# Optimization experiments

Hardware: AMD Instinct MI355X
Metric: run time of the kernel (lower is better)

## Reference

```python
import jax, jax.numpy as jnp
import numpy as np

NEG_SLOPE = 0.2


def gat_layer(x, adj, W, a_src, a_dst):
    # x: (C, in_dim), adj: (C, C) 0/1, W: (in_dim, H*D), a_src/a_dst: (H, D)
    C = x.shape[0]
    H, D = a_src.shape
    h = (x @ W).reshape(C, H, D)            # (C, H, D)
    hh = jnp.transpose(h, (1, 0, 2))        # (H, C, D)
    asrc = jnp.einsum('hcd,hd->hc', hh, a_src)  # (H, C)
    adst = jnp.einsum('hcd,hd->hc', hh, a_dst)  # (H, C)
    e = asrc[:, :, None] + adst[:, None, :]     # (H, C, C)
    e = jax.nn.leaky_relu(e, NEG_SLOPE)
    e = jnp.where(adj[None, :, :] == 0, -jnp.inf, e)
    attn = jax.nn.softmax(e, axis=-1)           # (H, C, C)
    out = jnp.einsum('hij,hjd->hid', attn, hh)  # (H, C, D)
    return jnp.transpose(out, (1, 0, 2)).reshape(C, H * D)


def setup_inputs() -> dict:
    key = jax.random.key(0)
    ks = jax.random.split(key, 12)
    B, doc_dim = 1024, 768
    C, label_dim = 4096, 768
    hidden, H = 512, 4
    D = hidden // H  # 128

    doc_x = jax.random.normal(ks[0], (B, doc_dim), dtype=jnp.float32)
    label_init = jax.random.normal(ks[1], (C, label_dim), dtype=jnp.float32)
    adj = jax.random.randint(ks[2], (C, C), 0, 2, dtype=jnp.int32)
    adj = adj.at[jnp.arange(C), jnp.arange(C)].set(1)  # self-loops

    def xavier(k, shape):
        fan_in, fan_out = shape[0], shape[1]
        lim = jnp.sqrt(6.0 / (fan_in + fan_out)).astype(jnp.float32)
        return jax.random.uniform(k, shape, jnp.float32, -lim, lim)

    W1 = xavier(ks[3], (label_dim, hidden))
    a_src1 = xavier(ks[4], (H, D))
    a_dst1 = xavier(ks[5], (H, D))
    W2 = xavier(ks[6], (hidden, hidden))
    a_src2 = xavier(ks[7], (H, D))
    a_dst2 = xavier(ks[8], (H, D))
    Wd = xavier(ks[9], (doc_dim, hidden))
    bd = jnp.zeros((hidden,), jnp.float32)
    return {"doc_x": doc_x, "label_init": label_init, "adj": adj,
            "W1": W1, "a_src1": a_src1, "a_dst1": a_dst1,
            "W2": W2, "a_src2": a_src2, "a_dst2": a_dst2,
            "Wd": Wd, "bd": bd}


def reference(doc_x, label_init, adj, W1, a_src1, a_dst1, W2, a_src2, a_dst2, Wd, bd):
    # doc_proj (dropout = identity in eval)
    doc_h = jax.nn.relu(doc_x @ Wd + bd)            # (B, hidden)
    # label encoder: GAT -> ELU -> GAT
    h = gat_layer(label_init, adj, W1, a_src1, a_dst1)
    h = jax.nn.elu(h)
    label_h = gat_layer(h, adj, W2, a_src2, a_dst2)  # (C, hidden)
    logits = doc_h @ label_h.T                      # (B, C)
    return logits
```

## Files before the change

### kernel.cpp

```cpp
#include <hip/hip_runtime.h>
#include <hip/hip_bf16.h>
#include <math.h>

#define BDOCS   1024
#define CNODES  4096
#define INDIM   768
#define HID     512
#define NHEAD   4
#define HDIM    128
#define NEG_SLOPE 0.2f

#define KSPLIT  8
#define JPER    (CNODES / KSPLIT)
#define NCH     (JPER / 32)

typedef __attribute__((ext_vector_type(8))) short short8;
typedef __attribute__((ext_vector_type(4))) float f32x4;

__device__ __forceinline__ float lrelu(float x) { return x > 0.f ? x : NEG_SLOPE * x; }

__device__ __forceinline__ short f2bf(float f) {
    union { float f; unsigned u; } v; v.f = f;
    unsigned r = (v.u + 0x7fff + ((v.u >> 16) & 1)) >> 16;
    return (short)r;
}
__device__ __forceinline__ float bf2f(short s) {
    union { float f; unsigned u; } v; v.u = ((unsigned)(unsigned short)s) << 16;
    return v.f;
}
__device__ __forceinline__ unsigned pk2(float a, float b) {
    union { float f; unsigned u; } x, y; x.f = a; y.f = b;
    unsigned lo = (x.u + 0x7fff + ((x.u >> 16) & 1)) >> 16;
    unsigned hi = (y.u + 0x7fff + ((y.u >> 16) & 1)) >> 16;
    return lo | (hi << 16);
}
__device__ __forceinline__ short hup(float f) {
    union { float f; unsigned u; } v; v.f = f;
    return (short)((v.u + 0x8000) >> 16);
}
__device__ __forceinline__ unsigned encf(float x) {
    union { float f; unsigned u; } v; v.f = x;
    return (v.u & 0x80000000u) ? ~v.u : (v.u | 0x80000000u);
}
__device__ __forceinline__ float decf(unsigned u) {
    union { float f; unsigned u; } v;
    v.u = (u & 0x80000000u) ? (u ^ 0x80000000u) : ~u;
    return v.f;
}

__device__ void frag_T_dev(const float* __restrict__ src, short* __restrict__ dst,
                           int N, int K, int jc, int nq, float (*tile)[132])
{
    const int t  = threadIdx.x;
    const int KC = K >> 5;
#pragma unroll
    for (int it = 0; it < 16; it++) {
        const int e = it * 256 + t;
        const int j = e >> 7, n = e & 127;
        tile[j][n] = src[(size_t)(jc * 32 + j) * N + nq * 128 + n];
    }
    __syncthreads();
#pragma unroll
    for (int s = 0; s < 2; s++) {
        const int item = s * 256 + t;
        const int nbl = item >> 6, lane = item & 63;
        const int nr = lane & 15, kq = lane >> 4;
        short8 v;
#pragma unroll
        for (int jr = 0; jr < 8; jr++)
            v[jr] = f2bf(tile[kq * 8 + jr][nbl * 16 + nr]);
        *(short8*)&dst[((size_t)((nq * 8 + nbl) * KC + jc) * 64 + lane) * 8] = v;
    }
}

__device__ void frag_A_dev(const float* __restrict__ src, short* __restrict__ dst,
                           int C, int rb, int cq, float (*tile)[132])
{
    const int t  = threadIdx.x;
    const int KC = C >> 5;
#pragma unroll
    for (int it = 0; it < 8; it++) {
        const int e = it * 256 + t;
        const int r = e >> 7, c = e & 127;
        tile[r][c] = src[(size_t)(rb * 16 + r) * C + cq * 128 + c];
    }
    __syncthreads();
    const int kcl = t >> 6, lane = t & 63;
    const int m = lane & 15, kq = lane >> 4;
    short8 v8;
#pragma unroll
    for (int j = 0; j < 8; j++) v8[j] = f2bf(tile[m][kcl * 32 + kq * 8 + j]);
    *(short8*)&dst[((size_t)(rb * KC + cq * 4 + kcl) * 64 + lane) * 8] = v8;
}

#define PREP_BLOCKS (65536 + 96 + 96 + 64 + 384 + 1536)
__global__ __launch_bounds__(256)
void prep_all(const int* __restrict__ adj, unsigned long long* __restrict__ adjb64,
              const float* __restrict__ Wd, short* __restrict__ Wdf,
              const float* __restrict__ W1, short* __restrict__ W1f,
              const float* __restrict__ W2, short* __restrict__ W2f,
              const float* __restrict__ doc_x, short* __restrict__ dxf,
              const float* __restrict__ label_init, short* __restrict__ lif,
              unsigned* __restrict__ MhEnc)
{
    __shared__ float tile[32][132];
    int b = blockIdx.x;
    if (b < 65536) {
        if (b == 0 && threadIdx.x < 16) MhEnc[threadIdx.x] = 0x007FFFFFu;
        const int t    = threadIdx.x;
        const int gw   = b * 4 + (t >> 6);
        const int lane = t & 63;
        const int i  = gw >> 6;
        const int j0 = (gw & 63) * 64;
        const int a  = adj[(size_t)i * CNODES + j0 + lane];
        const unsigned long long msk = __ballot(a != 0);
        if (lane == 0) adjb64[(size_t)i * 64 + (j0 >> 6)] = msk;
        return;
    }
    b -= 65536;
    if (b < 96)  { frag_T_dev(Wd, Wdf, HID, INDIM, b % 24, b / 24, tile); return; }
    b -= 96;
    if (b < 96)  { frag_T_dev(W1, W1f, HID, INDIM, b % 24, b / 24, tile); return; }
    b -= 96;
    if (b < 64)  { frag_T_dev(W2, W2f, HID, HID, b % 16, b / 16, tile); return; }
    b -= 64;
    if (b < 384) { frag_A_dev(doc_x, dxf, INDIM, b % 64, b / 64, tile); return; }
    b -= 384;
    frag_A_dev(label_init, lif, INDIM, b % 256, b / 256, tile);
}

template <int KC>
__global__ __launch_bounds__(64)
void gemm_hpre(const short* __restrict__ Af, const short* __restrict__ Bf,
               const float* __restrict__ a_src, const float* __restrict__ a_dst,
               short* __restrict__ hbTf, float* __restrict__ asrc, float* __restrict__ adst,
               unsigned* __restrict__ MhEncH)
{
    __shared__ __align__(16) short tileT[64][24];
    const int lane = threadIdx.x;
    const int mb   = blockIdx.x;
    const int h    = blockIdx.y >> 1;
    const int ch   = blockIdx.y & 1;
    const int i0   = mb * 16;

    f32x4 acc[4];
#pragma unroll
    for (int c = 0; c < 4; c++) acc[c] = (f32x4){0.f, 0.f, 0.f, 0.f};

    const short* ap = Af + (size_t)mb * KC * 512 + lane * 8;
    const short* bp = Bf + (size_t)(h * 8 + ch * 4) * KC * 512 + lane * 8;

#pragma unroll 2
    for (int kc = 0; kc < KC; kc++) {
        short8 a = *(const short8*)(ap + (size_t)kc * 512);
#pragma unroll
        for (int c = 0; c < 4; c++) {
            short8 bf = *(const short8*)(bp + ((size_t)c * KC + kc) * 512);
            acc[c] = __builtin_amdgcn_mfma_f32_16x16x32_bf16(a, bf, acc[c], 0, 0, 0);
        }
    }

    const int col = lane & 15, q4 = lane >> 4;

#pragma unroll
    for (int c = 0; c < 4; c++) {
        uint2 u;
        u.x = pk2(acc[c][0], acc[c][1]);
        u.y = pk2(acc[c][2], acc[c][3]);
        *(uint2*)&tileT[c * 16 + col][q4 * 4] = u;
    }
    __syncthreads();
    {
        const int jc = mb >> 1, khalf = mb & 1;
        const int nr = lane & 15, kq = lane >> 4;
        if ((kq >> 1) == khalf) {
#pragma unroll
            for (int cl = 0; cl < 4; cl++) {
                short8 v = *(const short8*)&tileT[cl * 16 + nr][(kq & 1) * 8];
                const int nbl = h * 8 + ch * 4 + cl;
                *(short8*)&hbTf[(((size_t)nbl * (CNODES / 32) + jc) * 64 + lane) * 8] = v;
            }
        }
    }

    float ssrc[4] = {}, sdst[4] = {};
#pragma unroll
    for (int c = 0; c < 4; c++) {
        const float vs = a_src[h * 128 + ch * 64 + c * 16 + col];
        const float vd = a_dst[h * 128 + ch * 64 + c * 16 + col];
#pragma unroll
        for (int r = 0; r < 4; r++) {
            ssrc[r] += acc[c][r] * vs;
            sdst[r] += acc[c][r] * vd;
        }
    }
#pragma unroll
    for (int mask = 1; mask <= 8; mask <<= 1)
#pragma unroll
        for (int r = 0; r < 4; r++) {
            ssrc[r] += __shfl_xor(ssrc[r], mask);
            sdst[r] += __shfl_xor(sdst[r], mask);
        }
    if (col == 0) {
#pragma unroll
        for (int r = 0; r < 4; r++) {
            const int row = i0 + q4 * 4 + r;
            atomicAdd(asrc + h * CNODES + row, ssrc[r]);
            atomicAdd(adst + h * CNODES + row, sdst[r]);
        }
    }
    float wmax = fmaxf(fmaxf(sdst[0], sdst[1]), fmaxf(sdst[2], sdst[3]));
    wmax = fmaxf(wmax, __shfl_xor(wmax, 16));
    wmax = fmaxf(wmax, __shfl_xor(wmax, 32));
    if (lane == 0) atomicMax(MhEncH + h * 2 + ch, encf(wmax));
}

template <int KC>
__global__ __launch_bounds__(64)
void gemm_doc(const short* __restrict__ Af, const short* __restrict__ Bf,
              const float* __restrict__ bias, short* __restrict__ dhf)
{
    __shared__ __align__(16) short tile[16][32];
    const int lane = threadIdx.x;
    const int mb = blockIdx.x;
    const int ng = blockIdx.y;

    f32x4 acc[2];
#pragma unroll
    for (int c = 0; c < 2; c++) acc[c] = (f32x4){0.f, 0.f, 0.f, 0.f};

    const short* ap = Af + (size_t)mb * KC * 512 + lane * 8;
    const short* bp = Bf + (size_t)(ng * 2) * KC * 512 + lane * 8;

#pragma unroll 2
    for (int kc = 0; kc < KC; kc++) {
        short8 a = *(const short8*)(ap + (size_t)kc * 512);
#pragma unroll
        for (int c = 0; c < 2; c++) {
            short8 bf = *(const short8*)(bp + ((size_t)c * KC + kc) * 512);
            acc[c] = __builtin_amdgcn_mfma_f32_16x16x32_bf16(a, bf, acc[c], 0, 0, 0);
        }
    }

    const int col = lane & 15, q4 = lane >> 4;
#pragma unroll
    for (int c = 0; c < 2; c++)
#pragma unroll
        for (int r = 0; r < 4; r++) {
            float v = fmaxf(acc[c][r] + bias[ng * 32 + c * 16 + col], 0.f);
            tile[q4 * 4 + r][c * 16 + col] = f2bf(v);
        }
    __syncthreads();
    const int m = lane & 15, kq = lane >> 4;
    short8 v = *(const short8*)&tile[m][kq * 8];
    *(short8*)&dhf[(((size_t)mb * 16 + ng) * 64 + lane) * 8] = v;
}

template <int KC>
__global__ __launch_bounds__(64)
void gemm_frag(const short* __restrict__ Af, const short* __restrict__ Bf,
               float* __restrict__ Cmat, int N)
{
    const int lane = threadIdx.x;
    const int mb0  = blockIdx.x * 2;
    const int ng   = blockIdx.y;

    f32x4 acc[2][4];
#pragma unroll
    for (int f = 0; f < 2; f++)
#pragma unroll
        for (int c = 0; c < 4; c++) acc[f][c] = (f32x4){0.f, 0.f, 0.f, 0.f};

    const short* ap0 = Af + (size_t)mb0 * KC * 512 + lane * 8;
    const short* ap1 = ap0 + (size_t)KC * 512;
    const short* bp  = Bf + (size_t)(ng * 4) * KC * 512 + lane * 8;

#pragma unroll 2
    for (int kc = 0; kc < KC; kc++) {
        short8 a0 = *(const short8*)(ap0 + (size_t)kc * 512);
        short8 a1 = *(const short8*)(ap1 + (size_t)kc * 512);
#pragma unroll
        for (int c = 0; c < 4; c++) {
            short8 bf = *(const short8*)(bp + ((size_t)c * KC + kc) * 512);
            acc[0][c] = __builtin_amdgcn_mfma_f32_16x16x32_bf16(a0, bf, acc[0][c], 0, 0, 0);
            acc[1][c] = __builtin_amdgcn_mfma_f32_16x16x32_bf16(a1, bf, acc[1][c], 0, 0, 0);
        }
    }

    const int col = lane & 15, q4 = lane >> 4;
#pragma unroll
    for (int f = 0; f < 2; f++)
#pragma unroll
        for (int c = 0; c < 4; c++)
#pragma unroll
            for (int r = 0; r < 4; r++) {
                const int row = (mb0 + f) * 16 + q4 * 4 + r;
                Cmat[(size_t)row * N + ng * 64 + c * 16 + col] = acc[f][c][r];
            }
}

__global__ __launch_bounds__(512, 2)
void attn_pv(const short* __restrict__ hbTf,
             const unsigned int* __restrict__ adjb,
             const float* __restrict__ asrc, const float* __restrict__ adst,
             const unsigned* __restrict__ MhEncH,
             short* __restrict__ part, float* __restrict__ lpart)
{
    __shared__ __align__(16) float E1s[NHEAD][512];
    __shared__ __align__(16) float E2s[NHEAD][512];
    __shared__ __align__(16) short tileO[32][520];

    const int t    = threadIdx.x;
    const int ww   = t >> 6;
    const int w    = ww & 3;
    const int f2   = ww >> 2;
    const int lane = t & 63;
    const int m    = lane & 15;
    const int kq   = lane >> 4;
    const int i0   = blockIdx.x * 64;
    const int iw   = i0 + f2 * 32;
    const int ks   = blockIdx.y;
    const int js   = ks * JPER;

    {
        const int j = js + t;
#pragma unroll
        for (int h = 0; h < NHEAD; h++) {
            const float mhh = decf(MhEncH[h * 2]) + decf(MhEncH[h * 2 + 1]);
            const float d = adst[h * CNODES + j] - mhh;
            E1s[h][t] = __expf(d);
            E2s[h][t] = __expf(0.2f * d);
        }
    }

    const float mh  = decf(MhEncH[w * 2]) + decf(MhEncH[w * 2 + 1]);
    const float as0 = asrc[w * CNODES + iw + m];
    const float as1 = asrc[w * CNODES + iw + 16 + m];
    const float mr0 = lrelu(as0 + mh), mr1 = lrelu(as1 + mh);
    const float A10 = __expf(as0 + mh - mr0),          A11 = __expf(as1 + mh - mr1);
    const float A20 = __expf(0.2f * (as0 + mh) - mr0), A21 = __expf(0.2f * (as1 + mh) - mr1);
    const float T00 = __expf(-as0 - mh),               T01 = __expf(-as1 - mh);

    f32x4 acc[2][8], accO[2];
#pragma unroll
    for (int f = 0; f < 2; f++) {
        accO[f] = (f32x4){0.f, 0.f, 0.f, 0.f};
#pragma unroll
        for (int c = 0; c < 8; c++) acc[f][c] = (f32x4){0.f, 0.f, 0.f, 0.f};
    }
    short8 ones;
#pragma unroll
    for (int q = 0; q < 8; q++) ones[q] = (short)0x3F80;

    const unsigned int* ar0 = adjb + (size_t)(iw + m) * 128 + ks * NCH;
    const unsigned int* ar1 = adjb + (size_t)(iw + 16 + m) * 128 + ks * NCH;

    __syncthreads();

#pragma unroll 2
    for (int ch = 0; ch < NCH; ch++) {
        const int jl = ch * 32;
        const unsigned int aw0 = ar0[ch] >> (kq * 8);
        const unsigned int aw1 = ar1[ch] >> (kq * 8);
        const float4 x0 = *(const float4*)&E1s[w][jl + kq * 8];
        const float4 x1 = *(const float4*)&E1s[w][jl + kq * 8 + 4];
        const float4 y0 = *(const float4*)&E2s[w][jl + kq * 8];
        const float4 y1 = *(const float4*)&E2s[w][jl + kq * 8 + 4];
        const float e1v[8] = {x0.x, x0.y, x0.z, x0.w, x1.x, x1.y, x1.z, x1.w};
        const float e2v[8] = {y0.x, y0.y, y0.z, y0.w, y1.x, y1.y, y1.z, y1.w};

        short8 a0, a1;
#pragma unroll
        for (int q = 0; q < 8; q++) {
            const float e1 = e1v[q], e2 = e2v[q];
            const bool c0 = e1 > T00, c1 = e1 > T01;
            float w0 = (c0 ? A10 : A20) * (c0 ? e1 : e2);
            float w1 = (c1 ? A11 : A21) * (c1 ? e1 : e2);
            w0 = ((aw0 >> q) & 1u) ? w0 : 0.f;
            w1 = ((aw1 >> q) & 1u) ? w1 : 0.f;
            a0[q] = hup(w0);
            a1[q] = hup(w1);
        }

        const short* bbase = hbTf + (((size_t)(w * 8) * 128 + ((js + jl) >> 5)) * 64 + lane) * 8;
#pragma unroll
        for (int c = 0; c < 8; c++) {
            short8 bf = *(const short8*)(bbase + (size_t)c * 128 * 64 * 8);
            acc[0][c] = __builtin_amdgcn_mfma_f32_16x16x32_bf16(a0, bf, acc[0][c], 0, 0, 0);
            acc[1][c] = __builtin_amdgcn_mfma_f32_16x16x32_bf16(a1, bf, acc[1][c], 0, 0, 0);
        }
        accO[0] = __builtin_amdgcn_mfma_f32_16x16x32_bf16(a0, ones, accO[0], 0, 0, 0);
        accO[1] = __builtin_amdgcn_mfma_f32_16x16x32_bf16(a1, ones, accO[1], 0, 0, 0);
    }

    if (m == 0) {
#pragma unroll
        for (int f = 0; f < 2; f++)
#pragma unroll
            for (int r = 0; r < 4; r++)
                lpart[((size_t)ks * NHEAD + w) * CNODES + iw + f * 16 + kq * 4 + r] = accO[f][r];
    }

    short* pS = part + (size_t)ks * CNODES * HID;
    for (int half = 0; half < 2; half++) {
        __syncthreads();
        if (f2 == half) {
#pragma unroll
            for (int f = 0; f < 2; f++)
#pragma unroll
                for (int c = 0; c < 8; c++)
#pragma unroll
                    for (int r = 0; r < 4; r++)
                        tileO[f * 16 + kq * 4 + r][w * 128 + c * 16 + m] = f2bf(acc[f][c][r]);
        }
        __syncthreads();
#pragma unroll
        for (int it = 0; it < 4; it++) {
            const int u   = it * 512 + t;
            const int row = u >> 6, un = u & 63;
            uint4 v = *(const uint4*)&tileO[row][un * 8];
            *(uint4*)&pS[(size_t)(i0 + half * 32 + row) * HID + un * 8] = v;
        }
    }
}

template <bool ELU>
__global__ __launch_bounds__(256)
void reduce_norm_frag(const short* __restrict__ part, const float* __restrict__ lpart,
                      short* __restrict__ dst)
{
    const int t = threadIdx.x;
    const int W = blockIdx.x * 4 + (t >> 6);
    const int lane = t & 63;
    const int rb = W >> 4, kc = W & 15;
    const int m = lane & 15, kq = lane >> 4;
    const int i = rb * 16 + m;
    const int n0 = kc * 32 + kq * 8;
    const int h = kc >> 2;

    float v[8] = {};
    float l = 0.f;
#pragma unroll
    for (int s = 0; s < KSPLIT; s++) {
        const uint4 raw = *(const uint4*)&part[(size_t)s * CNODES * HID + (size_t)i * HID + n0];
        const unsigned rr[4] = {raw.x, raw.y, raw.z, raw.w};
#pragma unroll
        for (int q = 0; q < 4; q++) {
            v[q * 2]     += bf2f((short)(rr[q] & 0xffff));
            v[q * 2 + 1] += bf2f((short)(rr[q] >> 16));
        }
        l += lpart[((size_t)s * NHEAD + h) * CNODES + i];
    }
    const float inv = 1.0f / l;
    short8 o;
#pragma unroll
    for (int q = 0; q < 8; q++) {
        float x = v[q] * inv;
        if (ELU) x = x > 0.f ? x : (__expf(x) - 1.f);
        o[q] = f2bf(x);
    }
    *(short8*)&dst[((size_t)(rb * 16 + kc) * 64 + lane) * 8] = o;
}

extern "C" void kernel_launch(void* const* d_in, const int* in_sizes, int n_in,
                              void* d_out, int out_size, void* d_ws, size_t ws_size,
                              hipStream_t stream)
{
    const float* doc_x      = (const float*)d_in[0];
    const float* label_init = (const float*)d_in[1];
    const int*   adj        = (const int*)d_in[2];
    const float* W1         = (const float*)d_in[3];
    const float* a_src1     = (const float*)d_in[4];
    const float* a_dst1     = (const float*)d_in[5];
    const float* W2         = (const float*)d_in[6];
    const float* a_src2     = (const float*)d_in[7];
    const float* a_dst2     = (const float*)d_in[8];
    const float* Wd         = (const float*)d_in[9];
    const float* bd         = (const float*)d_in[10];
    float*       out        = (float*)d_out;

    char* wsb = (char*)d_ws;
    size_t off = 0;
    auto alloc = [&](size_t bytes) -> char* {
        char* p = wsb + off;
        off = (off + bytes + 255) & ~(size_t)255;
        return p;
    };

    float* asrc  = (float*)alloc(NHEAD * CNODES * 4);
    float* adst  = (float*)alloc(NHEAD * CNODES * 4);
    unsigned* MhEncH = (unsigned*)alloc(256);
    float* lpart = (float*)alloc((size_t)KSPLIT * NHEAD * CNODES * 4);
    unsigned int* adjb = (unsigned int*)alloc((size_t)CNODES * 128 * 4);
    short* hbTf  = (short*)alloc((size_t)CNODES * HID * 2);
    short* Wdf   = (short*)alloc((size_t)INDIM * HID * 2);
    short* W1f   = (short*)alloc((size_t)INDIM * HID * 2);
    short* W2f   = (short*)alloc((size_t)HID * HID * 2);
    short* dxf   = (short*)alloc((size_t)BDOCS * INDIM * 2);
    short* Af_li = (short*)alloc((size_t)CNODES * INDIM * 2);
    short* Af2   = (short*)alloc((size_t)CNODES * HID * 2);
    short* lhf   = (short*)alloc((size_t)CNODES * HID * 2);
    short* dhf   = (short*)alloc((size_t)BDOCS * HID * 2);
    short* part  = (short*)alloc((size_t)KSPLIT * CNODES * HID * 2);
    (void)ws_size;

    const dim3 blk(256);

    hipMemsetAsync(asrc, 0, (size_t)2 * NHEAD * CNODES * 4, stream);

    prep_all<<<PREP_BLOCKS, blk, 0, stream>>>(adj, (unsigned long long*)adjb,
                                              Wd, Wdf, W1, W1f, W2, W2f,
                                              doc_x, dxf, label_init, Af_li, MhEncH);

    gemm_doc<INDIM / 32><<<dim3(BDOCS / 16, HID / 32), 64, 0, stream>>>(dxf, Wdf, bd, dhf);

    gemm_hpre<INDIM / 32><<<dim3(CNODES / 16, 2 * NHEAD), 64, 0, stream>>>(
        Af_li, W1f, a_src1, a_dst1, hbTf, asrc, adst, MhEncH);

    attn_pv<<<dim3(CNODES / 64, KSPLIT), 512, 0, stream>>>(
        hbTf, adjb, asrc, adst, MhEncH, part, lpart);
    reduce_norm_frag<true><<<CNODES * HID / 256 / 8, blk, 0, stream>>>(part, lpart, Af2);

    hipMemsetAsync(asrc, 0, (size_t)2 * NHEAD * CNODES * 4, stream);

    gemm_hpre<HID / 32><<<dim3(CNODES / 16, 2 * NHEAD), 64, 0, stream>>>(
        Af2, W2f, a_src2, a_dst2, hbTf, asrc, adst, MhEncH + 8);

    attn_pv<<<dim3(CNODES / 64, KSPLIT), 512, 0, stream>>>(
        hbTf, adjb, asrc, adst, MhEncH + 8, part, lpart);
    reduce_norm_frag<false><<<CNODES * HID / 256 / 8, blk, 0, stream>>>(part, lpart, lhf);

    gemm_frag<HID / 32><<<dim3(BDOCS / 32, CNODES / 64), 64, 0, stream>>>(dhf, lhf, out, CNODES);
}
```

Baseline: 356.3 us.

## Use byte adjacency masks and packed bf16 conversion in attention weight build

Replaces the 1-bit packed adjacency with a byte-per-edge mask (0xFF/0x00) that can be ANDed directly onto packed bf16 pairs using v_perm. Weight computation switches from a compare-and-select against a threshold to fmaxf of the two leaky-relu branches, with hardware v_cvt_pk_bf16_f32 packing. The prep kernel gets 4x fewer blocks by vectorized int4 loads. The cost is an 8x larger mask (16 MB) read by each attention pass instead of 2 MB, trading inner-loop ALU work for memory traffic.

```diff
diff --git a/kernel.cpp b/kernel.cpp
--- a/kernel.cpp
+++ b/kernel.cpp
@@ -34,10 +34,6 @@
     unsigned hi = (y.u + 0x7fff + ((y.u >> 16) & 1)) >> 16;
     return lo | (hi << 16);
 }
-__device__ __forceinline__ short hup(float f) {
-    union { float f; unsigned u; } v; v.f = f;
-    return (short)((v.u + 0x8000) >> 16);
-}
 __device__ __forceinline__ unsigned encf(float x) {
     union { float f; unsigned u; } v; v.f = x;
     return (v.u & 0x80000000u) ? ~v.u : (v.u | 0x80000000u);
@@ -93,9 +89,9 @@
     *(short8*)&dst[((size_t)(rb * KC + cq * 4 + kcl) * 64 + lane) * 8] = v8;
 }
 
-#define PREP_BLOCKS (65536 + 96 + 96 + 64 + 384 + 1536)
+#define PREP_BLOCKS (16384 + 96 + 96 + 64 + 384 + 1536)
 __global__ __launch_bounds__(256)
-void prep_all(const int* __restrict__ adj, unsigned long long* __restrict__ adjb64,
+void prep_all(const int* __restrict__ adj, unsigned char* __restrict__ bmask,
               const float* __restrict__ Wd, short* __restrict__ Wdf,
               const float* __restrict__ W1, short* __restrict__ W1f,
               const float* __restrict__ W2, short* __restrict__ W2f,
@@ -105,19 +101,18 @@
 {
     __shared__ float tile[32][132];
     int b = blockIdx.x;
-    if (b < 65536) {
+    if (b < 16384) {
         if (b == 0 && threadIdx.x < 16) MhEnc[threadIdx.x] = 0x007FFFFFu;
-        const int t    = threadIdx.x;
-        const int gw   = b * 4 + (t >> 6);
-        const int lane = t & 63;
-        const int i  = gw >> 6;
-        const int j0 = (gw & 63) * 64;
-        const int a  = adj[(size_t)i * CNODES + j0 + lane];
-        const unsigned long long msk = __ballot(a != 0);
-        if (lane == 0) adjb64[(size_t)i * 64 + (j0 >> 6)] = msk;
+        const int idx = b * 256 + threadIdx.x;
+        const uint4 a = ((const uint4*)adj)[idx];
+        const unsigned mm = (a.x ? 0xffu       : 0u)
+                          | (a.y ? 0xff00u     : 0u)
+                          | (a.z ? 0xff0000u   : 0u)
+                          | (a.w ? 0xff000000u : 0u);
+        ((unsigned*)bmask)[idx] = mm;
         return;
     }
-    b -= 65536;
+    b -= 16384;
     if (b < 96)  { frag_T_dev(Wd, Wdf, HID, INDIM, b % 24, b / 24, tile); return; }
     b -= 96;
     if (b < 96)  { frag_T_dev(W1, W1f, HID, INDIM, b % 24, b / 24, tile); return; }
@@ -301,7 +296,7 @@
 
 __global__ __launch_bounds__(512, 2)
 void attn_pv(const short* __restrict__ hbTf,
-             const unsigned int* __restrict__ adjb,
+             const unsigned char* __restrict__ bmask,
              const float* __restrict__ asrc, const float* __restrict__ adst,
              const unsigned* __restrict__ MhEncH,
              short* __restrict__ part, float* __restrict__ lpart)
@@ -334,12 +329,11 @@
     }
 
     const float mh  = decf(MhEncH[w * 2]) + decf(MhEncH[w * 2 + 1]);
-    const float as0 = asrc[w * CNODES + iw + m];
-    const float as1 = asrc[w * CNODES + iw + 16 + m];
-    const float mr0 = lrelu(as0 + mh), mr1 = lrelu(as1 + mh);
-    const float A10 = __expf(as0 + mh - mr0),          A11 = __expf(as1 + mh - mr1);
-    const float A20 = __expf(0.2f * (as0 + mh) - mr0), A21 = __expf(0.2f * (as1 + mh) - mr1);
-    const float T00 = __expf(-as0 - mh),               T01 = __expf(-as1 - mh);
+    const float s0  = asrc[w * CNODES + iw + m] + mh;
+    const float s1  = asrc[w * CNODES + iw + 16 + m] + mh;
+    const float mr0 = lrelu(s0), mr1 = lrelu(s1);
+    const float A10 = __expf(s0 - mr0),        A11 = __expf(s1 - mr1);
+    const float A20 = __expf(0.2f * s0 - mr0), A21 = __expf(0.2f * s1 - mr1);
 
     f32x4 acc[2][8], accO[2];
 #pragma unroll
@@ -352,35 +346,41 @@
 #pragma unroll
     for (int q = 0; q < 8; q++) ones[q] = (short)0x3F80;
 
-    const unsigned int* ar0 = adjb + (size_t)(iw + m) * 128 + ks * NCH;
-    const unsigned int* ar1 = adjb + (size_t)(iw + 16 + m) * 128 + ks * NCH;
+    const unsigned char* bR0 = bmask + (size_t)(iw + m) * CNODES + js + kq * 8;
+    const unsigned char* bR1 = bmask + (size_t)(iw + 16 + m) * CNODES + js + kq * 8;
 
     __syncthreads();
 
 #pragma unroll 2
     for (int ch = 0; ch < NCH; ch++) {
         const int jl = ch * 32;
-        const unsigned int aw0 = ar0[ch] >> (kq * 8);
-        const unsigned int aw1 = ar1[ch] >> (kq * 8);
+        const uint2 M0 = *(const uint2*)(bR0 + jl);
+        const uint2 M1 = *(const uint2*)(bR1 + jl);
         const float4 x0 = *(const float4*)&E1s[w][jl + kq * 8];
         const float4 x1 = *(const float4*)&E1s[w][jl + kq * 8 + 4];
         const float4 y0 = *(const float4*)&E2s[w][jl + kq * 8];
         const float4 y1 = *(const float4*)&E2s[w][jl + kq * 8 + 4];
-        const float e1v[8] = {x0.x, x0.y, x0.z, x0.w, x1.x, x1.y, x1.z, x1.w};
-        const float e2v[8] = {y0.x, y0.y, y0.z, y0.w, y1.x, y1.y, y1.z, y1.w};
-
-        short8 a0, a1;
-#pragma unroll
-        for (int q = 0; q < 8; q++) {
-            const float e1 = e1v[q], e2 = e2v[q];
-            const bool c0 = e1 > T00, c1 = e1 > T01;
-            float w0 = (c0 ? A10 : A20) * (c0 ? e1 : e2);
-            float w1 = (c1 ? A11 : A21) * (c1 ? e1 : e2);
-            w0 = ((aw0 >> q) & 1u) ? w0 : 0.f;
-            w1 = ((aw1 >> q) & 1u) ? w1 : 0.f;
-            a0[q] = hup(w0);
-            a1[q] = hup(w1);
-        }
+
+        uint4 au0, au1;
+#define WPAIR(A1c, A2c, e1a, e1b, e2a, e2b, Mw, sel, dstu)                        \
+        {                                                                         \
+            float wl = fmaxf((A1c) * (e1a), (A2c) * (e2a));                       \
+            float wh = fmaxf((A1c) * (e1b), (A2c) * (e2b));                       \
+            unsigned pk_;                                                         \
+            asm("v_cvt_pk_bf16_f32 %0, %1, %2" : "=v"(pk_) : "v"(wl), "v"(wh));   \
+            dstu = pk_ & __builtin_amdgcn_perm(Mw, Mw, sel);                      \
+        }
+        WPAIR(A10, A20, x0.x, x0.y, y0.x, y0.y, M0.x, 0x01010000u, au0.x);
+        WPAIR(A10, A20, x0.z, x0.w, y0.z, y0.w, M0.x, 0x03030202u, au0.y);
+        WPAIR(A10, A20, x1.x, x1.y, y1.x, y1.y, M0.y, 0x01010000u, au0.z);
+        WPAIR(A10, A20, x1.z, x1.w, y1.z, y1.w, M0.y, 0x03030202u, au0.w);
+        WPAIR(A11, A21, x0.x, x0.y, y0.x, y0.y, M1.x, 0x01010000u, au1.x);
+        WPAIR(A11, A21, x0.z, x0.w, y0.z, y0.w, M1.x, 0x03030202u, au1.y);
+        WPAIR(A11, A21, x1.x, x1.y, y1.x, y1.y, M1.y, 0x01010000u, au1.z);
+        WPAIR(A11, A21, x1.z, x1.w, y1.z, y1.w, M1.y, 0x03030202u, au1.w);
+#undef WPAIR
+        const short8 a0 = *(const short8*)&au0;
+        const short8 a1 = *(const short8*)&au1;
 
         const short* bbase = hbTf + (((size_t)(w * 8) * 128 + ((js + jl) >> 5)) * 64 + lane) * 8;
 #pragma unroll
@@ -491,7 +491,7 @@
     float* adst  = (float*)alloc(NHEAD * CNODES * 4);
     unsigned* MhEncH = (unsigned*)alloc(256);
     float* lpart = (float*)alloc((size_t)KSPLIT * NHEAD * CNODES * 4);
-    unsigned int* adjb = (unsigned int*)alloc((size_t)CNODES * 128 * 4);
+    unsigned char* bmask = (unsigned char*)alloc((size_t)CNODES * CNODES);
     short* hbTf  = (short*)alloc((size_t)CNODES * HID * 2);
     short* Wdf   = (short*)alloc((size_t)INDIM * HID * 2);
     short* W1f   = (short*)alloc((size_t)INDIM * HID * 2);
@@ -508,7 +508,7 @@
 
     hipMemsetAsync(asrc, 0, (size_t)2 * NHEAD * CNODES * 4, stream);
 
-    prep_all<<<PREP_BLOCKS, blk, 0, stream>>>(adj, (unsigned long long*)adjb,
+    prep_all<<<PREP_BLOCKS, blk, 0, stream>>>(adj, bmask,
                                               Wd, Wdf, W1, W1f, W2, W2f,
                                               doc_x, dxf, label_init, Af_li, MhEncH);
 
@@ -518,7 +518,7 @@
         Af_li, W1f, a_src1, a_dst1, hbTf, asrc, adst, MhEncH);
 
     attn_pv<<<dim3(CNODES / 64, KSPLIT), 512, 0, stream>>>(
-        hbTf, adjb, asrc, adst, MhEncH, part, lpart);
+        hbTf, bmask, asrc, adst, MhEncH, part, lpart);
     reduce_norm_frag<true><<<CNODES * HID / 256 / 8, blk, 0, stream>>>(part, lpart, Af2);
 
     hipMemsetAsync(asrc, 0, (size_t)2 * NHEAD * CNODES * 4, stream);
@@ -527,7 +527,7 @@
         Af2, W2f, a_src2, a_dst2, hbTf, asrc, adst, MhEncH + 8);
 
     attn_pv<<<dim3(CNODES / 64, KSPLIT), 512, 0, stream>>>(
-        hbTf, adjb, asrc, adst, MhEncH + 8, part, lpart);
+        hbTf, bmask, asrc, adst, MhEncH + 8, part, lpart);
     reduce_norm_frag<false><<<CNODES * HID / 256 / 8, blk, 0, stream>>>(part, lpart, lhf);
 
     gemm_frag<HID / 32><<<dim3(BDOCS / 32, CNODES / 64), 64, 0, stream>>>(dhf, lhf, out, CNODES);
```

New measurement: 420.5 us. +18.0%, slower.

## Halve attn_pv rows per wave, raise occupancy, use fmax weights and hardware bf16 pack

Applied to the files above, without the earlier changes.

Each wave in attn_pv now handles 16 destination rows instead of 32, so accumulator registers are halved and the launch bound targets 6 blocks per CU. The grid doubles to CNODES/32 blocks. The leaky-relu branch select is replaced by a max of the two exponential forms, which is valid because exp is monotonic. The weights are packed to bf16 with v_cvt_pk_bf16_f32 instead of manual rounding. The trade-off is that each B fragment loaded from global memory now feeds one MFMA instead of two, which doubles B-operand traffic per FLOP.

```diff
diff --git a/kernel.cpp b/kernel.cpp
--- a/kernel.cpp
+++ b/kernel.cpp
@@ -33,10 +33,6 @@
     unsigned lo = (x.u + 0x7fff + ((x.u >> 16) & 1)) >> 16;
     unsigned hi = (y.u + 0x7fff + ((y.u >> 16) & 1)) >> 16;
     return lo | (hi << 16);
-}
-__device__ __forceinline__ short hup(float f) {
-    union { float f; unsigned u; } v; v.f = f;
-    return (short)((v.u + 0x8000) >> 16);
 }
 __device__ __forceinline__ unsigned encf(float x) {
     union { float f; unsigned u; } v; v.f = x;
@@ -299,7 +295,7 @@
             }
 }
 
-__global__ __launch_bounds__(512, 2)
+__global__ __launch_bounds__(512, 6)
 void attn_pv(const short* __restrict__ hbTf,
              const unsigned int* __restrict__ adjb,
              const float* __restrict__ asrc, const float* __restrict__ adst,
@@ -313,12 +309,12 @@
     const int t    = threadIdx.x;
     const int ww   = t >> 6;
     const int w    = ww & 3;
-    const int f2   = ww >> 2;
+    const int ig   = ww >> 2;
     const int lane = t & 63;
     const int m    = lane & 15;
     const int kq   = lane >> 4;
-    const int i0   = blockIdx.x * 64;
-    const int iw   = i0 + f2 * 32;
+    const int i0   = blockIdx.x * 32;
+    const int iw   = i0 + ig * 16;
     const int ks   = blockIdx.y;
     const int js   = ks * JPER;
 
@@ -334,26 +330,20 @@
     }
 
     const float mh  = decf(MhEncH[w * 2]) + decf(MhEncH[w * 2 + 1]);
-    const float as0 = asrc[w * CNODES + iw + m];
-    const float as1 = asrc[w * CNODES + iw + 16 + m];
-    const float mr0 = lrelu(as0 + mh), mr1 = lrelu(as1 + mh);
-    const float A10 = __expf(as0 + mh - mr0),          A11 = __expf(as1 + mh - mr1);
-    const float A20 = __expf(0.2f * (as0 + mh) - mr0), A21 = __expf(0.2f * (as1 + mh) - mr1);
-    const float T00 = __expf(-as0 - mh),               T01 = __expf(-as1 - mh);
-
-    f32x4 acc[2][8], accO[2];
-#pragma unroll
-    for (int f = 0; f < 2; f++) {
-        accO[f] = (f32x4){0.f, 0.f, 0.f, 0.f};
-#pragma unroll
-        for (int c = 0; c < 8; c++) acc[f][c] = (f32x4){0.f, 0.f, 0.f, 0.f};
-    }
+    const float s0  = asrc[w * CNODES + iw + m] + mh;
+    const float mr0 = lrelu(s0);
+    const float A10 = __expf(s0 - mr0);
+    const float A20 = __expf(0.2f * s0 - mr0);
+
+    f32x4 acc[8], accO;
+    accO = (f32x4){0.f, 0.f, 0.f, 0.f};
+#pragma unroll
+    for (int c = 0; c < 8; c++) acc[c] = (f32x4){0.f, 0.f, 0.f, 0.f};
     short8 ones;
 #pragma unroll
     for (int q = 0; q < 8; q++) ones[q] = (short)0x3F80;
 
     const unsigned int* ar0 = adjb + (size_t)(iw + m) * 128 + ks * NCH;
-    const unsigned int* ar1 = adjb + (size_t)(iw + 16 + m) * 128 + ks * NCH;
 
     __syncthreads();
 
@@ -361,7 +351,6 @@
     for (int ch = 0; ch < NCH; ch++) {
         const int jl = ch * 32;
         const unsigned int aw0 = ar0[ch] >> (kq * 8);
-        const unsigned int aw1 = ar1[ch] >> (kq * 8);
         const float4 x0 = *(const float4*)&E1s[w][jl + kq * 8];
         const float4 x1 = *(const float4*)&E1s[w][jl + kq * 8 + 4];
         const float4 y0 = *(const float4*)&E2s[w][jl + kq * 8];
@@ -369,58 +358,50 @@
         const float e1v[8] = {x0.x, x0.y, x0.z, x0.w, x1.x, x1.y, x1.z, x1.w};
         const float e2v[8] = {y0.x, y0.y, y0.z, y0.w, y1.x, y1.y, y1.z, y1.w};
 
-        short8 a0, a1;
+        float wv[8];
 #pragma unroll
         for (int q = 0; q < 8; q++) {
-            const float e1 = e1v[q], e2 = e2v[q];
-            const bool c0 = e1 > T00, c1 = e1 > T01;
-            float w0 = (c0 ? A10 : A20) * (c0 ? e1 : e2);
-            float w1 = (c1 ? A11 : A21) * (c1 ? e1 : e2);
-            w0 = ((aw0 >> q) & 1u) ? w0 : 0.f;
-            w1 = ((aw1 >> q) & 1u) ? w1 : 0.f;
-            a0[q] = hup(w0);
-            a1[q] = hup(w1);
-        }
+            float v = fmaxf(A10 * e1v[q], A20 * e2v[q]);
+            wv[q] = ((aw0 >> q) & 1u) ? v : 0.f;
+        }
+        uint4 au;
+#pragma unroll
+        for (int p = 0; p < 4; p++) {
+            unsigned pk_;
+            asm("v_cvt_pk_bf16_f32 %0, %1, %2"
+                : "=v"(pk_) : "v"(wv[p * 2]), "v"(wv[p * 2 + 1]));
+            ((unsigned*)&au)[p] = pk_;
+        }
+        const short8 a0 = *(const short8*)&au;
 
         const short* bbase = hbTf + (((size_t)(w * 8) * 128 + ((js + jl) >> 5)) * 64 + lane) * 8;
 #pragma unroll
         for (int c = 0; c < 8; c++) {
             short8 bf = *(const short8*)(bbase + (size_t)c * 128 * 64 * 8);
-            acc[0][c] = __builtin_amdgcn_mfma_f32_16x16x32_bf16(a0, bf, acc[0][c], 0, 0, 0);
-            acc[1][c] = __builtin_amdgcn_mfma_f32_16x16x32_bf16(a1, bf, acc[1][c], 0, 0, 0);
-        }
-        accO[0] = __builtin_amdgcn_mfma_f32_16x16x32_bf16(a0, ones, accO[0], 0, 0, 0);
-        accO[1] = __builtin_amdgcn_mfma_f32_16x16x32_bf16(a1, ones, accO[1], 0, 0, 0);
+            acc[c] = __builtin_amdgcn_mfma_f32_16x16x32_bf16(a0, bf, acc[c], 0, 0, 0);
+        }
+        accO = __builtin_amdgcn_mfma_f32_16x16x32_bf16(a0, ones, accO, 0, 0, 0);
     }
 
     if (m == 0) {
 #pragma unroll
-        for (int f = 0; f < 2; f++)
-#pragma unroll
-            for (int r = 0; r < 4; r++)
-                lpart[((size_t)ks * NHEAD + w) * CNODES + iw + f * 16 + kq * 4 + r] = accO[f][r];
-    }
-
+        for (int r = 0; r < 4; r++)
+            lpart[((size_t)ks * NHEAD + w) * CNODES + iw + kq * 4 + r] = accO[r];
+    }
+
+#pragma unroll
+    for (int c = 0; c < 8; c++)
+#pragma unroll
+        for (int r = 0; r < 4; r++)
+            tileO[ig * 16 + kq * 4 + r][w * 128 + c * 16 + m] = f2bf(acc[c][r]);
+    __syncthreads();
     short* pS = part + (size_t)ks * CNODES * HID;
-    for (int half = 0; half < 2; half++) {
-        __syncthreads();
-        if (f2 == half) {
-#pragma unroll
-            for (int f = 0; f < 2; f++)
-#pragma unroll
-                for (int c = 0; c < 8; c++)
-#pragma unroll
-                    for (int r = 0; r < 4; r++)
-                        tileO[f * 16 + kq * 4 + r][w * 128 + c * 16 + m] = f2bf(acc[f][c][r]);
-        }
-        __syncthreads();
-#pragma unroll
-        for (int it = 0; it < 4; it++) {
-            const int u   = it * 512 + t;
-            const int row = u >> 6, un = u & 63;
-            uint4 v = *(const uint4*)&tileO[row][un * 8];
-            *(uint4*)&pS[(size_t)(i0 + half * 32 + row) * HID + un * 8] = v;
-        }
+#pragma unroll
+    for (int it = 0; it < 4; it++) {
+        const int u   = it * 512 + t;
+        const int row = u >> 6, un = u & 63;
+        uint4 v = *(const uint4*)&tileO[row][un * 8];
+        *(uint4*)&pS[(size_t)(i0 + row) * HID + un * 8] = v;
     }
 }
 
@@ -517,7 +498,7 @@
     gemm_hpre<INDIM / 32><<<dim3(CNODES / 16, 2 * NHEAD), 64, 0, stream>>>(
         Af_li, W1f, a_src1, a_dst1, hbTf, asrc, adst, MhEncH);
 
-    attn_pv<<<dim3(CNODES / 64, KSPLIT), 512, 0, stream>>>(
+    attn_pv<<<dim3(CNODES / 32, KSPLIT), 512, 0, stream>>>(
         hbTf, adjb, asrc, adst, MhEncH, part, lpart);
     reduce_norm_frag<true><<<CNODES * HID / 256 / 8, blk, 0, stream>>>(part, lpart, Af2);
 
@@ -526,7 +507,7 @@
     gemm_hpre<HID / 32><<<dim3(CNODES / 16, 2 * NHEAD), 64, 0, stream>>>(
         Af2, W2f, a_src2, a_dst2, hbTf, asrc, adst, MhEncH + 8);
 
-    attn_pv<<<dim3(CNODES / 64, KSPLIT), 512, 0, stream>>>(
+    attn_pv<<<dim3(CNODES / 32, KSPLIT), 512, 0, stream>>>(
         hbTf, adjb, asrc, adst, MhEncH + 8, part, lpart);
     reduce_norm_frag<false><<<CNODES * HID / 256 / 8, blk, 0, stream>>>(part, lpart, lhf);
 
```

Measured after the change: 435.2 us. 1.22x slower.
